# Performance work log

Measured on AMD Instinct MI355X. Metric: run time of the kernel, lower is better.

## Reference

```python
import jax, jax.numpy as jnp
import numpy as np

B, N, D = 4, 4096, 512
H = 8
HD = D // H  # 64


def setup_inputs() -> dict:
    key = jax.random.key(0)
    ks = jax.random.split(key, 9)
    s = 1.0 / np.sqrt(D)
    return {
        "x": jax.random.normal(ks[0], (B, N, D), dtype=jnp.float32),
        "Wq": jax.random.normal(ks[1], (D, D), dtype=jnp.float32) * s,
        "bq": jax.random.normal(ks[2], (D,), dtype=jnp.float32) * 0.01,
        "Wk": jax.random.normal(ks[3], (D, D), dtype=jnp.float32) * s,
        "bk": jax.random.normal(ks[4], (D,), dtype=jnp.float32) * 0.01,
        "Wv": jax.random.normal(ks[5], (D, D), dtype=jnp.float32) * s,
        "bv": jax.random.normal(ks[6], (D,), dtype=jnp.float32) * 0.01,
        "Wo": jax.random.normal(ks[7], (D, D), dtype=jnp.float32) * s,
        "bo": jax.random.normal(ks[8], (D,), dtype=jnp.float32) * 0.01,
    }


def reference(x, Wq, bq, Wk, bk, Wv, bv, Wo, bo):
    # projections -> [B, H, N, HD]
    def split_heads(t):
        return t.reshape(B, N, H, HD).transpose(0, 2, 1, 3)

    q = split_heads(x @ Wq.T + bq)
    k = split_heads(x @ Wk.T + bk)
    v = split_heads(x @ Wv.T + bv)

    scale = 1.0 / np.sqrt(HD).astype(np.float32)
    scores = jnp.einsum("bhqd,bhkd->bhqk", q, k) * scale  # [B,H,N,N]
    attn = jax.nn.softmax(scores, axis=-1)
    out = jnp.einsum("bhqk,bhkd->bhqd", attn, v)  # [B,H,N,HD]
    out = out.transpose(0, 2, 1, 3).reshape(B, N, D)
    return out @ Wo.T + bo
```

## Files before the change

### kernel.cpp

```cpp
#include <hip/hip_runtime.h>
#include <hip/hip_bf16.h>

#define BB 4
#define NN 4096
#define DD 512
#define HH 8
#define HD 64

typedef __attribute__((ext_vector_type(4))) float f32x4;
typedef __attribute__((ext_vector_type(16))) float f32x16;
typedef __attribute__((ext_vector_type(8))) short short8;
typedef __attribute__((ext_vector_type(4))) unsigned int uint4v;

static __device__ __forceinline__ unsigned short f2bf(float f) {
    unsigned int u = __float_as_uint(f);
    u += 0x7fff + ((u >> 16) & 1);
    return (unsigned short)(u >> 16);
}

__global__ void convert_bf16(const float* __restrict__ in,
                             unsigned short* __restrict__ out, int n) {
    int i = (blockIdx.x * blockDim.x + threadIdx.x) * 8;
    int stride = gridDim.x * blockDim.x * 8;
    for (; i + 7 < n; i += stride) {
        f32x4 a = *reinterpret_cast<const f32x4*>(in + i);
        f32x4 b = *reinterpret_cast<const f32x4*>(in + i + 4);
        short8 o;
        o[0] = (short)f2bf(a[0]); o[1] = (short)f2bf(a[1]);
        o[2] = (short)f2bf(a[2]); o[3] = (short)f2bf(a[3]);
        o[4] = (short)f2bf(b[0]); o[5] = (short)f2bf(b[1]);
        o[6] = (short)f2bf(b[2]); o[7] = (short)f2bf(b[3]);
        *reinterpret_cast<short8*>(out + i) = o;
    }
}

__global__ void convert_weights(const float* __restrict__ W0, const float* __restrict__ W1,
                                const float* __restrict__ W2, const float* __restrict__ W3,
                                unsigned short* __restrict__ out) {
    int which = blockIdx.x >> 7;
    const float* src = which == 0 ? W0 : which == 1 ? W1 : which == 2 ? W2 : W3;
    unsigned short* dst = out + (size_t)which * DD * DD;
    int i = ((blockIdx.x & 127) * blockDim.x + threadIdx.x) * 8;
    f32x4 a = *reinterpret_cast<const f32x4*>(src + i);
    f32x4 b = *reinterpret_cast<const f32x4*>(src + i + 4);
    short8 o;
    o[0] = (short)f2bf(a[0]); o[1] = (short)f2bf(a[1]);
    o[2] = (short)f2bf(a[2]); o[3] = (short)f2bf(a[3]);
    o[4] = (short)f2bf(b[0]); o[5] = (short)f2bf(b[1]);
    o[6] = (short)f2bf(b[2]); o[7] = (short)f2bf(b[3]);
    *reinterpret_cast<short8*>(dst + i) = o;
}

template <int OUT_BF16>
__device__ __forceinline__
void gemm_tile(const unsigned short* __restrict__ A,
               const unsigned short* __restrict__ W,
               const float* __restrict__ bias,
               void* __restrict__ Cout, float scale,
               int brow, int bcol, uint4* ldsA, uint4* ldsB) {
    const int t = threadIdx.x;
    const int lane = t & 63;
    const int w = t >> 6;
    const int wr = w >> 1, wc = w & 1;
    const int l16 = lane & 15;
    const int lq = lane >> 4;

    f32x4 acc[4][4] = {};

    const int sr = t >> 1;
    const int c16 = (t & 1) * 2;

    for (int k0 = 0; k0 < 512; k0 += 32) {
        const uint4* gA = reinterpret_cast<const uint4*>(A + (size_t)(brow + sr) * 512 + k0 + c16 * 8);
        const uint4* gB = reinterpret_cast<const uint4*>(W + (size_t)(bcol + sr) * 512 + k0 + c16 * 8);
        uint4 a0 = gA[0], a1 = gA[1];
        uint4 b0 = gB[0], b1 = gB[1];
        __syncthreads();
        ldsA[(sr * 4 + c16) ^ (sr & 7)]     = a0;
        ldsA[(sr * 4 + c16 + 1) ^ (sr & 7)] = a1;
        ldsB[(sr * 4 + c16) ^ (sr & 7)]     = b0;
        ldsB[(sr * 4 + c16 + 1) ^ (sr & 7)] = b1;
        __syncthreads();
        short8 af[4], bfr[4];
#pragma unroll
        for (int m = 0; m < 4; ++m) {
            int ra = wr * 64 + m * 16 + l16;
            af[m] = *reinterpret_cast<short8*>(&ldsA[(ra * 4 + lq) ^ (ra & 7)]);
            int rb = wc * 64 + m * 16 + l16;
            bfr[m] = *reinterpret_cast<short8*>(&ldsB[(rb * 4 + lq) ^ (rb & 7)]);
        }
#pragma unroll
        for (int m = 0; m < 4; ++m)
#pragma unroll
            for (int n = 0; n < 4; ++n)
                acc[m][n] = __builtin_amdgcn_mfma_f32_16x16x32_bf16(af[m], bfr[n], acc[m][n], 0, 0, 0);
    }

#pragma unroll
    for (int m = 0; m < 4; ++m) {
        int row = brow + wr * 64 + m * 16 + lq * 4;
#pragma unroll
        for (int n = 0; n < 4; ++n) {
            int col = bcol + wc * 64 + n * 16 + l16;
            float bv = bias[col];
#pragma unroll
            for (int r = 0; r < 4; ++r) {
                float v = (acc[m][n][r] + bv) * scale;
                if (OUT_BF16) {
                    ((unsigned short*)Cout)[(size_t)(row + r) * 512 + col] = f2bf(v);
                } else {
                    ((float*)Cout)[(size_t)(row + r) * 512 + col] = v;
                }
            }
        }
    }
}

__global__ __launch_bounds__(256)
void gemm_qkv(const unsigned short* __restrict__ xb,
              const unsigned short* __restrict__ Wall,
              const float* __restrict__ bq, const float* __restrict__ bk,
              const float* __restrict__ bv,
              unsigned short* __restrict__ Qb, unsigned short* __restrict__ Kb,
              unsigned short* __restrict__ Vb, float cl) {
    __shared__ uint4 ldsA[128 * 4];
    __shared__ uint4 ldsB[128 * 4];
    int z = blockIdx.z;
    const unsigned short* W = Wall + (size_t)z * DD * DD;
    const float* bias = z == 0 ? bq : z == 1 ? bk : bv;
    unsigned short* dst = z == 0 ? Qb : z == 1 ? Kb : Vb;
    float scale = z == 0 ? cl : 1.0f;
    gemm_tile<1>(xb, W, bias, dst, scale,
                 (int)blockIdx.y * 128, (int)blockIdx.x * 128, ldsA, ldsB);
}

__global__ __launch_bounds__(256)
void gemm_bias_f32(const unsigned short* __restrict__ A,
                   const unsigned short* __restrict__ W,
                   const float* __restrict__ bias,
                   float* __restrict__ Cout) {
    __shared__ uint4 ldsA[128 * 4];
    __shared__ uint4 ldsB[128 * 4];
    gemm_tile<0>(A, W, bias, Cout, 1.0f,
                 (int)blockIdx.y * 128, (int)blockIdx.x * 128, ldsA, ldsB);
}

__global__ __launch_bounds__(256)
void transpose_v(const unsigned short* __restrict__ Vb, unsigned short* __restrict__ Vt) {
    __shared__ unsigned short tile[64][72];
    const int bh = blockIdx.y;
    const int b = bh >> 3, h = bh & 7;
    const int n0 = blockIdx.x * 64;
    const int t = threadIdx.x;
    {
        int r = t >> 2;
        int cs = (t & 3) * 16;
        const short8* src = reinterpret_cast<const short8*>(
            Vb + (size_t)(b * NN + n0 + r) * DD + h * HD + cs);
        short8 v0 = src[0], v1 = src[1];
#pragma unroll
        for (int j = 0; j < 8; ++j) {
            tile[r][cs + j]     = (unsigned short)v0[j];
            tile[r][cs + 8 + j] = (unsigned short)v1[j];
        }
    }
    __syncthreads();
    {
        int d = t >> 2;
        int ns = (t & 3) * 16;
        short8 o0, o1;
#pragma unroll
        for (int j = 0; j < 8; ++j) {
            o0[j] = (short)tile[ns + j][d];
            o1[j] = (short)tile[ns + 8 + j][d];
        }
        unsigned short* dst = Vt + ((size_t)bh * HD + d) * NN + n0 + ns;
        *reinterpret_cast<short8*>(dst)     = o0;
        *reinterpret_cast<short8*>(dst + 8) = o1;
    }
}

__global__ __launch_bounds__(512)
void flash_attn(const unsigned short* __restrict__ Qb,
                const unsigned short* __restrict__ Kb,
                const unsigned short* __restrict__ Vt,
                unsigned short* __restrict__ Ob) {
    __shared__ __align__(16) char lds[32768];
    const int t = threadIdx.x;
    const int lane = t & 63;
    const int w = t >> 6;
    const int nid = (blockIdx.x & 7) * 64 + (blockIdx.x >> 3);
    const int bh = nid >> 4;
    const int qb = nid & 15;
    const int b = bh >> 3, h = bh & 7;
    const int q0 = qb * 256 + w * 32;
    const int l32 = lane & 31;
    const int hi = lane >> 5;

    const int i8 = lane >> 3, g8 = lane & 7;

    const unsigned short* qptr = Qb + (size_t)(b * NN + q0 + l32) * DD + h * HD + hi * 8;
    short8 qf[4];
#pragma unroll
    for (int c = 0; c < 4; ++c)
        qf[c] = *reinterpret_cast<const short8*>(qptr + c * 16);

    const f32x16 Z = {};
    f32x16 OT0 = {}, OT1 = {};
    float lsx = 0.f, lsy = 0.f;

    int koff[8], voff[8];
#pragma unroll
    for (int sub = 0; sub < 2; ++sub) {
#pragma unroll
        for (int c = 0; c < 4; ++c) {
            int row = sub * 32 + l32;
            int g = (hi + 2 * c) ^ (row & 7) ^ ((row >> 3) & 7);
            koff[sub * 4 + c] = row * 128 + g * 16;
        }
#pragma unroll
        for (int dblk = 0; dblk < 2; ++dblk)
#pragma unroll
            for (int c2 = 0; c2 < 2; ++c2) {
                int row = dblk * 32 + l32;
                int g = ((sub << 2) + (c2 << 1) + hi) ^ (row & 7) ^ ((row >> 3) & 7);
                voff[sub * 4 + dblk * 2 + c2] = 8192 + row * 128 + g * 16;
            }
    }

    const int rowl = w * 8 + i8;
    const int gsw = (g8 ^ i8 ^ (w & 7)) * 8;
    const unsigned short* kp = Kb + (size_t)(b * NN + rowl) * DD + h * HD + gsw;
    const unsigned short* vp = Vt + ((size_t)bh * HD + rowl) * NN + gsw;

    auto STAGE = [&](int bb) {
        __builtin_amdgcn_global_load_lds(
            (const __attribute__((address_space(1))) void*)kp,
            (__attribute__((address_space(3))) void*)(lds + bb + w * 1024), 16, 0, 0);
        __builtin_amdgcn_global_load_lds(
            (const __attribute__((address_space(1))) void*)vp,
            (__attribute__((address_space(3))) void*)(lds + bb + 8192 + w * 1024), 16, 0, 0);
        kp += 64 * DD; vp += 64;
    };

    auto softpack = [&](const f32x16& S, short8& pa, short8& pb) {
        unsigned int wq[8];
#pragma unroll
        for (int j = 0; j < 8; ++j) {
            float p0 = __builtin_exp2f(S[2 * j]);
            float p1 = __builtin_exp2f(S[2 * j + 1]);
            lsx += p0; lsy += p1;
            asm("v_cvt_pk_bf16_f32 %0, %1, %2" : "=v"(wq[j]) : "v"(p0), "v"(p1));
        }
        asm("v_permlane32_swap_b32 %0, %1" : "+v"(wq[0]), "+v"(wq[2]));
        asm("v_permlane32_swap_b32 %0, %1" : "+v"(wq[1]), "+v"(wq[3]));
        asm("v_permlane32_swap_b32 %0, %1" : "+v"(wq[4]), "+v"(wq[6]));
        asm("v_permlane32_swap_b32 %0, %1" : "+v"(wq[5]), "+v"(wq[7]));
        uint4v pu0 = {wq[0], wq[1], wq[2], wq[3]};
        uint4v pu1 = {wq[4], wq[5], wq[6], wq[7]};
        pa = __builtin_bit_cast(short8, pu0);
        pb = __builtin_bit_cast(short8, pu1);
    };

    auto COMPUTE = [&](int BO) {
        short8 kf[8];
#pragma unroll
        for (int i = 0; i < 8; ++i)
            kf[i] = *reinterpret_cast<const short8*>(lds + BO + koff[i]);

        f32x16 S0, S1;
        S0 = __builtin_amdgcn_mfma_f32_32x32x16_bf16(kf[0], qf[0], Z, 0, 0, 0);
        S1 = __builtin_amdgcn_mfma_f32_32x32x16_bf16(kf[4], qf[0], Z, 0, 0, 0);
        S0 = __builtin_amdgcn_mfma_f32_32x32x16_bf16(kf[1], qf[1], S0, 0, 0, 0);
        S1 = __builtin_amdgcn_mfma_f32_32x32x16_bf16(kf[5], qf[1], S1, 0, 0, 0);
        S0 = __builtin_amdgcn_mfma_f32_32x32x16_bf16(kf[2], qf[2], S0, 0, 0, 0);
        S1 = __builtin_amdgcn_mfma_f32_32x32x16_bf16(kf[6], qf[2], S1, 0, 0, 0);
        S0 = __builtin_amdgcn_mfma_f32_32x32x16_bf16(kf[3], qf[3], S0, 0, 0, 0);
        S1 = __builtin_amdgcn_mfma_f32_32x32x16_bf16(kf[7], qf[3], S1, 0, 0, 0);

        short8 vf[8];
#pragma unroll
        for (int i = 0; i < 8; ++i)
            vf[i] = *reinterpret_cast<const short8*>(lds + BO + voff[i]);

        short8 p0a, p0b, p1a, p1b;
        softpack(S0, p0a, p0b);
        OT0 = __builtin_amdgcn_mfma_f32_32x32x16_bf16(vf[0], p0a, OT0, 0, 0, 0);
        OT0 = __builtin_amdgcn_mfma_f32_32x32x16_bf16(vf[1], p0b, OT0, 0, 0, 0);
        OT1 = __builtin_amdgcn_mfma_f32_32x32x16_bf16(vf[2], p0a, OT1, 0, 0, 0);
        OT1 = __builtin_amdgcn_mfma_f32_32x32x16_bf16(vf[3], p0b, OT1, 0, 0, 0);
        softpack(S1, p1a, p1b);
        OT0 = __builtin_amdgcn_mfma_f32_32x32x16_bf16(vf[4], p1a, OT0, 0, 0, 0);
        OT0 = __builtin_amdgcn_mfma_f32_32x32x16_bf16(vf[5], p1b, OT0, 0, 0, 0);
        OT1 = __builtin_amdgcn_mfma_f32_32x32x16_bf16(vf[6], p1a, OT1, 0, 0, 0);
        OT1 = __builtin_amdgcn_mfma_f32_32x32x16_bf16(vf[7], p1b, OT1, 0, 0, 0);
    };

    STAGE(0);
    asm volatile("s_waitcnt vmcnt(0)" ::: "memory");
    __builtin_amdgcn_s_barrier();
    asm volatile("" ::: "memory");

    for (int it = 0; it < 32; ++it) {
        STAGE(16384);
        asm volatile("s_waitcnt vmcnt(2)" ::: "memory");
        __builtin_amdgcn_s_barrier();
        asm volatile("" ::: "memory");
        COMPUTE(0);
        asm volatile("" ::: "memory");
        __builtin_amdgcn_s_barrier();
        asm volatile("" ::: "memory");
        if (it != 31) {
            STAGE(0);
            asm volatile("s_waitcnt vmcnt(2)" ::: "memory");
        } else {
            asm volatile("s_waitcnt vmcnt(0)" ::: "memory");
        }
        __builtin_amdgcn_s_barrier();
        asm volatile("" ::: "memory");
        COMPUTE(16384);
        if (it != 31) {
            asm volatile("" ::: "memory");
            __builtin_amdgcn_s_barrier();
            asm volatile("" ::: "memory");
        }
    }

    float lsum = lsx + lsy;
    lsum += __shfl_xor(lsum, 32);
    float inv = 1.0f / lsum;
    char* lw = lds + w * 4096;
#pragma unroll
    for (int dblk = 0; dblk < 2; ++dblk) {
#pragma unroll
        for (int g = 0; g < 4; ++g) {
#pragma unroll
            for (int j = 0; j < 2; ++j) {
                int r = 4 * g + 2 * j;
                int d = dblk * 32 + 8 * g + 2 * j + 4 * hi;
                float a = (dblk ? OT1[r] : OT0[r]) * inv;
                float bqv = (dblk ? OT1[r + 1] : OT0[r + 1]) * inv;
                unsigned int wv;
                asm("v_cvt_pk_bf16_f32 %0, %1, %2" : "=v"(wv) : "v"(a), "v"(bqv));
                int addr = (l32 * 128 + d * 2) ^ ((l32 & 7) << 4);
                *reinterpret_cast<unsigned int*>(lw + addr) = wv;
            }
        }
    }
#pragma unroll
    for (int it = 0; it < 4; ++it) {
        int q = lane >> 1;
        int seg = (lane & 1) + it * 2;
        uint4 val = *reinterpret_cast<uint4*>(lw + ((q * 128 + seg * 16) ^ ((q & 7) << 4)));
        *reinterpret_cast<uint4*>(Ob + (size_t)(b * NN + q0 + q) * DD + h * HD + seg * 8) = val;
    }
}

extern "C" void kernel_launch(void* const* d_in, const int* in_sizes, int n_in,
                              void* d_out, int out_size, void* d_ws, size_t ws_size,
                              hipStream_t stream) {
    (void)in_sizes; (void)n_in; (void)out_size; (void)ws_size;
    const float* x  = (const float*)d_in[0];
    const float* Wq = (const float*)d_in[1];
    const float* bq = (const float*)d_in[2];
    const float* Wk = (const float*)d_in[3];
    const float* bk = (const float*)d_in[4];
    const float* Wv = (const float*)d_in[5];
    const float* bv = (const float*)d_in[6];
    const float* Wo = (const float*)d_in[7];
    const float* bo = (const float*)d_in[8];
    float* out = (float*)d_out;

    char* ws = (char*)d_ws;
    const size_t BUF = 16777216;
    unsigned short* xb  = (unsigned short*)(ws);
    unsigned short* Qb  = (unsigned short*)(ws + BUF);
    unsigned short* Kb  = (unsigned short*)(ws + 2 * BUF);
    unsigned short* Vb  = (unsigned short*)(ws + 3 * BUF);
    unsigned short* Wqb = (unsigned short*)(ws + 4 * BUF);
    unsigned short* Wob = Wqb + 3 * 262144;
    unsigned short* Vt  = xb;
    unsigned short* Ob  = Vb;

    const int NTOK = BB * NN;
    const float cl = 0.125f * 1.4426950408889634f;

    convert_bf16<<<2048, 256, 0, stream>>>(x, xb, NTOK * DD);
    convert_weights<<<512, 256, 0, stream>>>(Wq, Wk, Wv, Wo, Wqb);

    dim3 ggrid(4, NTOK / 128, 3);
    gemm_qkv<<<ggrid, 256, 0, stream>>>(xb, Wqb, bq, bk, bv, Qb, Kb, Vb, cl);

    transpose_v<<<dim3(NN / 64, BB * HH), 256, 0, stream>>>(Vb, Vt);

    flash_attn<<<512, 512, 0, stream>>>(Qb, Kb, Vt, Ob);

    gemm_bias_f32<<<dim3(4, NTOK / 128), 256, 0, stream>>>(Ob, Wob, bo, out);
}
```

Baseline: 274.8 us.

## Process two 32-query blocks per wave to reuse K/V fragments in flash attention

Each wave now computes 64 query rows (two 32-row blocks A and B) against every staged K/V tile. Each K and V fragment read from LDS then feeds two MFMAs instead of one, and the grid is halved to 256 blocks. The QK product of the second key half is interleaved with the PV MFMAs of the first half so that softmax work overlaps with matrix ops. The cost is more accumulator registers and half as many resident waves, which may reduce latency hiding.

```diff
diff --git a/kernel.cpp b/kernel.cpp
--- a/kernel.cpp
+++ b/kernel.cpp
@@ -189,25 +189,28 @@
     const int t = threadIdx.x;
     const int lane = t & 63;
     const int w = t >> 6;
-    const int nid = (blockIdx.x & 7) * 64 + (blockIdx.x >> 3);
-    const int bh = nid >> 4;
-    const int qb = nid & 15;
+    const int nid = (blockIdx.x & 7) * 32 + (blockIdx.x >> 3);
+    const int bh = nid >> 3;
+    const int qb = nid & 7;
     const int b = bh >> 3, h = bh & 7;
-    const int q0 = qb * 256 + w * 32;
+    const int q0 = qb * 512 + w * 64;
     const int l32 = lane & 31;
     const int hi = lane >> 5;
 
     const int i8 = lane >> 3, g8 = lane & 7;
 
-    const unsigned short* qptr = Qb + (size_t)(b * NN + q0 + l32) * DD + h * HD + hi * 8;
-    short8 qf[4];
-#pragma unroll
-    for (int c = 0; c < 4; ++c)
-        qf[c] = *reinterpret_cast<const short8*>(qptr + c * 16);
+    const unsigned short* qptrA = Qb + (size_t)(b * NN + q0 + l32) * DD + h * HD + hi * 8;
+    const unsigned short* qptrB = qptrA + (size_t)32 * DD;
+    short8 qfA[4], qfB[4];
+#pragma unroll
+    for (int c = 0; c < 4; ++c) {
+        qfA[c] = *reinterpret_cast<const short8*>(qptrA + c * 16);
+        qfB[c] = *reinterpret_cast<const short8*>(qptrB + c * 16);
+    }
 
     const f32x16 Z = {};
-    f32x16 OT0 = {}, OT1 = {};
-    float lsx = 0.f, lsy = 0.f;
+    f32x16 OT0A = {}, OT1A = {}, OT0B = {}, OT1B = {};
+    float lsA = 0.f, lsB = 0.f;
 
     int koff[8], voff[8];
 #pragma unroll
@@ -243,13 +246,13 @@
         kp += 64 * DD; vp += 64;
     };
 
-    auto softpack = [&](const f32x16& S, short8& pa, short8& pb) {
+    auto softpack = [&](const f32x16& S, short8& pa, short8& pb, float& ls) {
         unsigned int wq[8];
 #pragma unroll
         for (int j = 0; j < 8; ++j) {
             float p0 = __builtin_exp2f(S[2 * j]);
             float p1 = __builtin_exp2f(S[2 * j + 1]);
-            lsx += p0; lsy += p1;
+            ls += p0 + p1;
             asm("v_cvt_pk_bf16_f32 %0, %1, %2" : "=v"(wq[j]) : "v"(p0), "v"(p1));
         }
         asm("v_permlane32_swap_b32 %0, %1" : "+v"(wq[0]), "+v"(wq[2]));
@@ -263,37 +266,65 @@
     };
 
     auto COMPUTE = [&](int BO) {
-        short8 kf[8];
-#pragma unroll
-        for (int i = 0; i < 8; ++i)
-            kf[i] = *reinterpret_cast<const short8*>(lds + BO + koff[i]);
-
-        f32x16 S0, S1;
-        S0 = __builtin_amdgcn_mfma_f32_32x32x16_bf16(kf[0], qf[0], Z, 0, 0, 0);
-        S1 = __builtin_amdgcn_mfma_f32_32x32x16_bf16(kf[4], qf[0], Z, 0, 0, 0);
-        S0 = __builtin_amdgcn_mfma_f32_32x32x16_bf16(kf[1], qf[1], S0, 0, 0, 0);
-        S1 = __builtin_amdgcn_mfma_f32_32x32x16_bf16(kf[5], qf[1], S1, 0, 0, 0);
-        S0 = __builtin_amdgcn_mfma_f32_32x32x16_bf16(kf[2], qf[2], S0, 0, 0, 0);
-        S1 = __builtin_amdgcn_mfma_f32_32x32x16_bf16(kf[6], qf[2], S1, 0, 0, 0);
-        S0 = __builtin_amdgcn_mfma_f32_32x32x16_bf16(kf[3], qf[3], S0, 0, 0, 0);
-        S1 = __builtin_amdgcn_mfma_f32_32x32x16_bf16(kf[7], qf[3], S1, 0, 0, 0);
-
-        short8 vf[8];
-#pragma unroll
-        for (int i = 0; i < 8; ++i)
-            vf[i] = *reinterpret_cast<const short8*>(lds + BO + voff[i]);
-
-        short8 p0a, p0b, p1a, p1b;
-        softpack(S0, p0a, p0b);
-        OT0 = __builtin_amdgcn_mfma_f32_32x32x16_bf16(vf[0], p0a, OT0, 0, 0, 0);
-        OT0 = __builtin_amdgcn_mfma_f32_32x32x16_bf16(vf[1], p0b, OT0, 0, 0, 0);
-        OT1 = __builtin_amdgcn_mfma_f32_32x32x16_bf16(vf[2], p0a, OT1, 0, 0, 0);
-        OT1 = __builtin_amdgcn_mfma_f32_32x32x16_bf16(vf[3], p0b, OT1, 0, 0, 0);
-        softpack(S1, p1a, p1b);
-        OT0 = __builtin_amdgcn_mfma_f32_32x32x16_bf16(vf[4], p1a, OT0, 0, 0, 0);
-        OT0 = __builtin_amdgcn_mfma_f32_32x32x16_bf16(vf[5], p1b, OT0, 0, 0, 0);
-        OT1 = __builtin_amdgcn_mfma_f32_32x32x16_bf16(vf[6], p1a, OT1, 0, 0, 0);
-        OT1 = __builtin_amdgcn_mfma_f32_32x32x16_bf16(vf[7], p1b, OT1, 0, 0, 0);
+        short8 kf0 = *reinterpret_cast<const short8*>(lds + BO + koff[0]);
+        short8 kf1 = *reinterpret_cast<const short8*>(lds + BO + koff[1]);
+        short8 kf2 = *reinterpret_cast<const short8*>(lds + BO + koff[2]);
+        short8 kf3 = *reinterpret_cast<const short8*>(lds + BO + koff[3]);
+        f32x16 SA, SB;
+        SA = __builtin_amdgcn_mfma_f32_32x32x16_bf16(kf0, qfA[0], Z, 0, 0, 0);
+        SB = __builtin_amdgcn_mfma_f32_32x32x16_bf16(kf0, qfB[0], Z, 0, 0, 0);
+        SA = __builtin_amdgcn_mfma_f32_32x32x16_bf16(kf1, qfA[1], SA, 0, 0, 0);
+        SB = __builtin_amdgcn_mfma_f32_32x32x16_bf16(kf1, qfB[1], SB, 0, 0, 0);
+        SA = __builtin_amdgcn_mfma_f32_32x32x16_bf16(kf2, qfA[2], SA, 0, 0, 0);
+        SB = __builtin_amdgcn_mfma_f32_32x32x16_bf16(kf2, qfB[2], SB, 0, 0, 0);
+        SA = __builtin_amdgcn_mfma_f32_32x32x16_bf16(kf3, qfA[3], SA, 0, 0, 0);
+        SB = __builtin_amdgcn_mfma_f32_32x32x16_bf16(kf3, qfB[3], SB, 0, 0, 0);
+
+        short8 vf0 = *reinterpret_cast<const short8*>(lds + BO + voff[0]);
+        short8 vf1 = *reinterpret_cast<const short8*>(lds + BO + voff[1]);
+        short8 vf2 = *reinterpret_cast<const short8*>(lds + BO + voff[2]);
+        short8 vf3 = *reinterpret_cast<const short8*>(lds + BO + voff[3]);
+        short8 kg0 = *reinterpret_cast<const short8*>(lds + BO + koff[4]);
+        short8 kg1 = *reinterpret_cast<const short8*>(lds + BO + koff[5]);
+        short8 kg2 = *reinterpret_cast<const short8*>(lds + BO + koff[6]);
+        short8 kg3 = *reinterpret_cast<const short8*>(lds + BO + koff[7]);
+
+        short8 pA0, pA1, pB0, pB1;
+        softpack(SA, pA0, pA1, lsA);
+        softpack(SB, pB0, pB1, lsB);
+
+        f32x16 SC, SD;
+        SC = __builtin_amdgcn_mfma_f32_32x32x16_bf16(kg0, qfA[0], Z, 0, 0, 0);
+        SD = __builtin_amdgcn_mfma_f32_32x32x16_bf16(kg0, qfB[0], Z, 0, 0, 0);
+        OT0A = __builtin_amdgcn_mfma_f32_32x32x16_bf16(vf0, pA0, OT0A, 0, 0, 0);
+        OT0B = __builtin_amdgcn_mfma_f32_32x32x16_bf16(vf0, pB0, OT0B, 0, 0, 0);
+        SC = __builtin_amdgcn_mfma_f32_32x32x16_bf16(kg1, qfA[1], SC, 0, 0, 0);
+        SD = __builtin_amdgcn_mfma_f32_32x32x16_bf16(kg1, qfB[1], SD, 0, 0, 0);
+        OT0A = __builtin_amdgcn_mfma_f32_32x32x16_bf16(vf1, pA1, OT0A, 0, 0, 0);
+        OT0B = __builtin_amdgcn_mfma_f32_32x32x16_bf16(vf1, pB1, OT0B, 0, 0, 0);
+        SC = __builtin_amdgcn_mfma_f32_32x32x16_bf16(kg2, qfA[2], SC, 0, 0, 0);
+        SD = __builtin_amdgcn_mfma_f32_32x32x16_bf16(kg2, qfB[2], SD, 0, 0, 0);
+        OT1A = __builtin_amdgcn_mfma_f32_32x32x16_bf16(vf2, pA0, OT1A, 0, 0, 0);
+        OT1B = __builtin_amdgcn_mfma_f32_32x32x16_bf16(vf2, pB0, OT1B, 0, 0, 0);
+        SC = __builtin_amdgcn_mfma_f32_32x32x16_bf16(kg3, qfA[3], SC, 0, 0, 0);
+        SD = __builtin_amdgcn_mfma_f32_32x32x16_bf16(kg3, qfB[3], SD, 0, 0, 0);
+        OT1A = __builtin_amdgcn_mfma_f32_32x32x16_bf16(vf3, pA1, OT1A, 0, 0, 0);
+        OT1B = __builtin_amdgcn_mfma_f32_32x32x16_bf16(vf3, pB1, OT1B, 0, 0, 0);
+
+        short8 vg0 = *reinterpret_cast<const short8*>(lds + BO + voff[4]);
+        short8 vg1 = *reinterpret_cast<const short8*>(lds + BO + voff[5]);
+        short8 vg2 = *reinterpret_cast<const short8*>(lds + BO + voff[6]);
+        short8 vg3 = *reinterpret_cast<const short8*>(lds + BO + voff[7]);
+        softpack(SC, pA0, pA1, lsA);
+        softpack(SD, pB0, pB1, lsB);
+        OT0A = __builtin_amdgcn_mfma_f32_32x32x16_bf16(vg0, pA0, OT0A, 0, 0, 0);
+        OT0B = __builtin_amdgcn_mfma_f32_32x32x16_bf16(vg0, pB0, OT0B, 0, 0, 0);
+        OT0A = __builtin_amdgcn_mfma_f32_32x32x16_bf16(vg1, pA1, OT0A, 0, 0, 0);
+        OT0B = __builtin_amdgcn_mfma_f32_32x32x16_bf16(vg1, pB1, OT0B, 0, 0, 0);
+        OT1A = __builtin_amdgcn_mfma_f32_32x32x16_bf16(vg2, pA0, OT1A, 0, 0, 0);
+        OT1B = __builtin_amdgcn_mfma_f32_32x32x16_bf16(vg2, pB0, OT1B, 0, 0, 0);
+        OT1A = __builtin_amdgcn_mfma_f32_32x32x16_bf16(vg3, pA1, OT1A, 0, 0, 0);
+        OT1B = __builtin_amdgcn_mfma_f32_32x32x16_bf16(vg3, pB1, OT1B, 0, 0, 0);
     };
 
     STAGE(0);
@@ -326,33 +357,39 @@
         }
     }
 
-    float lsum = lsx + lsy;
-    lsum += __shfl_xor(lsum, 32);
-    float inv = 1.0f / lsum;
     char* lw = lds + w * 4096;
 #pragma unroll
-    for (int dblk = 0; dblk < 2; ++dblk) {
-#pragma unroll
-        for (int g = 0; g < 4; ++g) {
-#pragma unroll
-            for (int j = 0; j < 2; ++j) {
-                int r = 4 * g + 2 * j;
-                int d = dblk * 32 + 8 * g + 2 * j + 4 * hi;
-                float a = (dblk ? OT1[r] : OT0[r]) * inv;
-                float bqv = (dblk ? OT1[r + 1] : OT0[r + 1]) * inv;
-                unsigned int wv;
-                asm("v_cvt_pk_bf16_f32 %0, %1, %2" : "=v"(wv) : "v"(a), "v"(bqv));
-                int addr = (l32 * 128 + d * 2) ^ ((l32 & 7) << 4);
-                *reinterpret_cast<unsigned int*>(lw + addr) = wv;
+    for (int qblk = 0; qblk < 2; ++qblk) {
+        float ls = qblk ? lsB : lsA;
+        ls += __shfl_xor(ls, 32);
+        float inv = 1.0f / ls;
+        const f32x16& O0 = qblk ? OT0B : OT0A;
+        const f32x16& O1 = qblk ? OT1B : OT1A;
+#pragma unroll
+        for (int dblk = 0; dblk < 2; ++dblk) {
+#pragma unroll
+            for (int g = 0; g < 4; ++g) {
+#pragma unroll
+                for (int j = 0; j < 2; ++j) {
+                    int r = 4 * g + 2 * j;
+                    int d = dblk * 32 + 8 * g + 2 * j + 4 * hi;
+                    float a = (dblk ? O1[r] : O0[r]) * inv;
+                    float bqv = (dblk ? O1[r + 1] : O0[r + 1]) * inv;
+                    unsigned int wv;
+                    asm("v_cvt_pk_bf16_f32 %0, %1, %2" : "=v"(wv) : "v"(a), "v"(bqv));
+                    int addr = (l32 * 128 + d * 2) ^ ((l32 & 7) << 4);
+                    *reinterpret_cast<unsigned int*>(lw + addr) = wv;
+                }
             }
         }
-    }
-#pragma unroll
-    for (int it = 0; it < 4; ++it) {
-        int q = lane >> 1;
-        int seg = (lane & 1) + it * 2;
-        uint4 val = *reinterpret_cast<uint4*>(lw + ((q * 128 + seg * 16) ^ ((q & 7) << 4)));
-        *reinterpret_cast<uint4*>(Ob + (size_t)(b * NN + q0 + q) * DD + h * HD + seg * 8) = val;
+        int qg0 = q0 + qblk * 32;
+#pragma unroll
+        for (int it = 0; it < 4; ++it) {
+            int q = lane >> 1;
+            int seg = (lane & 1) + it * 2;
+            uint4 val = *reinterpret_cast<uint4*>(lw + ((q * 128 + seg * 16) ^ ((q & 7) << 4)));
+            *reinterpret_cast<uint4*>(Ob + (size_t)(b * NN + qg0 + q) * DD + h * HD + seg * 8) = val;
+        }
     }
 }
 
@@ -393,7 +430,7 @@
 
     transpose_v<<<dim3(NN / 64, BB * HH), 256, 0, stream>>>(Vb, Vt);
 
-    flash_attn<<<512, 512, 0, stream>>>(Qb, Kb, Vt, Ob);
+    flash_attn<<<256, 512, 0, stream>>>(Qb, Kb, Vt, Ob);
 
     gemm_bias_f32<<<dim3(4, NTOK / 128), 256, 0, stream>>>(Ob, Wob, bo, out);
 }
```

Measured after the change: 306.0 us. +11.3%, slower.
